# Optimization experiments

Hardware: AMD Instinct MI355X
Metric: run time of the kernel (lower is better)

The kernel has to match this reference:

```python
import jax, jax.numpy as jnp
import numpy as np

MARGIN = 0.5
EPS = 1e-6  # torch F.pairwise_distance adds eps to the difference before the norm
B, N, D = 1024, 1024, 64


def setup_inputs() -> dict:
    key = jax.random.key(0)
    ka, kp, kn = jax.random.split(key, 3)
    anchor = jax.random.normal(ka, (B, N, D), dtype=jnp.float32)
    positive = jax.random.normal(kp, (B, N, D), dtype=jnp.float32)
    negative = jax.random.normal(kn, (B, N, D), dtype=jnp.float32)
    return {"anchor": anchor, "positive": positive, "negative": negative}


def reference(anchor, positive, negative):
    # pairwise L2 distances over the feature dim -> [B, N]
    dist_pos = jnp.linalg.norm(anchor - positive + EPS, axis=-1)
    dist_neg = jnp.linalg.norm(anchor - negative + EPS, axis=-1)

    # hard-negative mining, vectorized over the batch:
    # candidates are columns where dist_pos - dist_neg + margin > 0;
    # among candidates pick the column with the LARGEST dist_neg
    diff = dist_pos - dist_neg + MARGIN            # [B, N]
    valid = diff > 0                               # [B, N]
    neg_scores = jnp.where(valid, dist_neg, -jnp.inf)
    sel_col = jnp.argmax(neg_scores, axis=1)       # [B] column index of hard negative

    # faithful to the original: negative is indexed on its FIRST dim with the
    # selected column index (requires B == N), yielding [B, N, D]
    hard_neg = negative[sel_col]
    has_valid = jnp.any(valid, axis=1)             # rows the original would keep

    loss = jnp.mean(jax.nn.relu(MARGIN + dist_pos - dist_neg))
    return loss, hard_neg, has_valid
```

## Files before the change

### kernel.cpp

```cpp
#include <hip/hip_runtime.h>
#include <math.h>

#define BB 1024
#define NN 1024
#define DD 64
#define MARGIN_V 0.5f
#define EPS_V 1e-6f
#define QSPLIT 8
#define QCOLS (NN / QSPLIT)

typedef float f32x4 __attribute__((ext_vector_type(4)));

__global__ __launch_bounds__(256) void k_dist(const float* __restrict__ a,
                                              const float* __restrict__ p,
                                              const float* __restrict__ g,
                                              float* __restrict__ ws_loss,
                                              float* __restrict__ ws_score,
                                              int* __restrict__ ws_idx,
                                              int* __restrict__ ws_valid)
{
    const int blk  = blockIdx.x;
    const int b    = blk >> 3;
    const int q    = blk & 7;
    const int tid  = threadIdx.x;
    const int lane = tid & 63;
    const int wave = tid >> 6;
    const int grp  = lane >> 4;
    const int gl   = lane & 15;
    const int group = wave * 4 + grp;

    const size_t base  = (size_t)b * (NN * DD);
    const int    ncol0 = q * QCOLS + group;
    const size_t off00 = base + (size_t)ncol0 * DD + (size_t)gl * 4;

    float loss_acc   = 0.f;
    float best_score = -INFINITY;
    int   best_idx   = 0;
    int   any_valid  = 0;

    f32x4 cA0 = __builtin_nontemporal_load((const f32x4*)(a + off00));
    f32x4 cP0 = __builtin_nontemporal_load((const f32x4*)(p + off00));
    f32x4 cG0 = *(const f32x4*)(g + off00);
    f32x4 cA1 = __builtin_nontemporal_load((const f32x4*)(a + off00 + 16 * DD));
    f32x4 cP1 = __builtin_nontemporal_load((const f32x4*)(p + off00 + 16 * DD));
    f32x4 cG1 = *(const f32x4*)(g + off00 + 16 * DD);

    #pragma unroll
    for (int j = 0; j < 4; ++j) {
        f32x4 nA0, nP0, nG0, nA1, nP1, nG1;
        if (j < 3) {
            const size_t offn = off00 + (size_t)((j + 1) * 32) * DD;
            nA0 = __builtin_nontemporal_load((const f32x4*)(a + offn));
            nP0 = __builtin_nontemporal_load((const f32x4*)(p + offn));
            nG0 = *(const f32x4*)(g + offn);
            nA1 = __builtin_nontemporal_load((const f32x4*)(a + offn + 16 * DD));
            nP1 = __builtin_nontemporal_load((const f32x4*)(p + offn + 16 * DD));
            nG1 = *(const f32x4*)(g + offn + 16 * DD);
        }

        const int n0 = ncol0 + j * 32;
        const int n1 = n0 + 16;

        float dp0 = 0.f, dn0 = 0.f, dp1 = 0.f, dn1 = 0.f, t;
        #pragma unroll
        for (int e = 0; e < 4; ++e) {
            t = cA0[e] - cP0[e] + EPS_V; dp0 += t * t;
            t = cA0[e] - cG0[e] + EPS_V; dn0 += t * t;
            t = cA1[e] - cP1[e] + EPS_V; dp1 += t * t;
            t = cA1[e] - cG1[e] + EPS_V; dn1 += t * t;
        }

        for (int m = 1; m < 16; m <<= 1) {
            dp0 += __shfl_xor(dp0, m, 64);
            dn0 += __shfl_xor(dn0, m, 64);
            dp1 += __shfl_xor(dp1, m, 64);
            dn1 += __shfl_xor(dn1, m, 64);
        }

        if (gl == 0) {
            {
                const float diff = MARGIN_V + sqrtf(dp0) - sqrtf(dn0);
                loss_acc += fmaxf(diff, 0.f);
                const bool valid = diff > 0.f;
                any_valid |= (int)valid;
                const float score = valid ? sqrtf(dn0) : -INFINITY;
                if (score > best_score) { best_score = score; best_idx = n0; }
            }
            {
                const float diff = MARGIN_V + sqrtf(dp1) - sqrtf(dn1);
                loss_acc += fmaxf(diff, 0.f);
                const bool valid = diff > 0.f;
                any_valid |= (int)valid;
                const float score = valid ? sqrtf(dn1) : -INFINITY;
                if (score > best_score) { best_score = score; best_idx = n1; }
            }
        }

        if (j < 3) {
            cA0 = nA0; cP0 = nP0; cG0 = nG0;
            cA1 = nA1; cP1 = nP1; cG1 = nG1;
        }
    }

    __shared__ float s_score[16];
    __shared__ int   s_idx[16];
    __shared__ float s_loss[16];
    __shared__ int   s_valid[16];
    if (gl == 0) {
        s_score[group] = best_score;
        s_idx[group]   = best_idx;
        s_loss[group]  = loss_acc;
        s_valid[group] = any_valid;
    }
    __syncthreads();
    if (tid == 0) {
        float bs = s_score[0]; int bi = s_idx[0];
        float ls = s_loss[0];  int av = s_valid[0];
        for (int k = 1; k < 16; ++k) {
            const float sc = s_score[k]; const int ix = s_idx[k];
            if (sc > bs || (sc == bs && ix < bi)) { bs = sc; bi = ix; }
            ls += s_loss[k];
            av |= s_valid[k];
        }
        ws_loss[blk]  = ls;
        ws_score[blk] = bs;
        ws_idx[blk]   = bi;
        ws_valid[blk] = av;
    }
}

__global__ __launch_bounds__(1024) void k_merge(const float* __restrict__ ws_loss,
                                                const float* __restrict__ ws_score,
                                                const int* __restrict__ ws_idx,
                                                const int* __restrict__ ws_valid,
                                                float* __restrict__ out_loss,
                                                int* __restrict__ ws_sel,
                                                float* __restrict__ out_hasvalid)
{
    const int b = threadIdx.x;
    float ls = 0.f;
    float bs = -INFINITY;
    int   bi = 0x7fffffff;
    int   av = 0;
    for (int qq = 0; qq < QSPLIT; ++qq) {
        const int idx = b * QSPLIT + qq;
        const float sc = ws_score[idx];
        const int   ix = ws_idx[idx];
        if (sc > bs || (sc == bs && ix < bi)) { bs = sc; bi = ix; }
        ls += ws_loss[idx];
        av |= ws_valid[idx];
    }
    ws_sel[b] = bi;
    out_hasvalid[b] = av ? 1.0f : 0.0f;

    __shared__ float s[16];
    float v = ls;
    for (int m = 1; m < 64; m <<= 1) v += __shfl_xor(v, m, 64);
    if ((b & 63) == 0) s[b >> 6] = v;
    __syncthreads();
    if (b == 0) {
        float tot = 0.f;
        for (int k = 0; k < 16; ++k) tot += s[k];
        out_loss[0] = tot / (float)((size_t)BB * NN);
    }
}

__global__ __launch_bounds__(256) void k_gather(const float* __restrict__ g,
                                                const int* __restrict__ ws_sel,
                                                float* __restrict__ out_hn)
{
    const int b   = blockIdx.y;
    const int sel = ws_sel[b];
    const float* __restrict__ src = g      + (size_t)sel * (NN * DD);
    float* __restrict__       dst = out_hn + (size_t)b   * (NN * DD);
    const int t = blockIdx.x * blockDim.x + threadIdx.x;
    #pragma unroll
    for (int k = 0; k < (NN * DD) / 8192; ++k) {
        const int idx = t + k * 8192;
        __builtin_nontemporal_store(src[idx], dst + idx);
    }
}

extern "C" void kernel_launch(void* const* d_in, const int* in_sizes, int n_in,
                              void* d_out, int out_size, void* d_ws, size_t ws_size,
                              hipStream_t stream) {
    const float* anchor   = (const float*)d_in[0];
    const float* positive = (const float*)d_in[1];
    const float* negative = (const float*)d_in[2];
    float* out = (float*)d_out;

    float* out_loss     = out;
    float* out_hard_neg = out + 1;
    float* out_hasvalid = out + 1 + (size_t)BB * NN * DD;

    float* ws_loss  = (float*)d_ws;
    float* ws_score = ws_loss + BB * QSPLIT;
    int*   ws_idx   = (int*)(ws_score + BB * QSPLIT);
    int*   ws_valid = ws_idx + BB * QSPLIT;
    int*   ws_sel   = ws_valid + BB * QSPLIT;

    k_dist<<<dim3(BB * QSPLIT), dim3(256), 0, stream>>>(anchor, positive, negative,
                                                        ws_loss, ws_score, ws_idx, ws_valid);
    k_merge<<<dim3(1), dim3(1024), 0, stream>>>(ws_loss, ws_score, ws_idx, ws_valid,
                                                out_loss, ws_sel, out_hasvalid);
    k_gather<<<dim3(32, BB), dim3(256), 0, stream>>>(negative, ws_sel, out_hard_neg);
}
```

Baseline: 223.2 us.

## Map one thread per column in distance kernel and halve the column split

The distance kernel now gives each thread one whole 64-float row. The thread reads that row with sixteen 16-byte loads and reduces it locally, where before a 16-lane group split the row and reduced it with shuffles. The split per batch row drops from 8 blocks to 4, and the argmax/loss reduction becomes a wave-wide shuffle reduction. The valid flag is now derived from the best score. The aim is to remove the per-column cross-lane shuffle work. The cost is that each load instruction now has lanes strided 256 bytes apart, which hurts coalescing in a kernel that is bound by memory bandwidth.

```diff
diff --git a/kernel.cpp b/kernel.cpp
--- a/kernel.cpp
+++ b/kernel.cpp
@@ -6,7 +6,7 @@
 #define DD 64
 #define MARGIN_V 0.5f
 #define EPS_V 1e-6f
-#define QSPLIT 8
+#define QSPLIT 4
 #define QCOLS (NN / QSPLIT)
 
 typedef float f32x4 __attribute__((ext_vector_type(4)));
@@ -19,113 +19,85 @@
                                               int* __restrict__ ws_idx,
                                               int* __restrict__ ws_valid)
 {
-    const int blk  = blockIdx.x;
-    const int b    = blk >> 3;
-    const int q    = blk & 7;
-    const int tid  = threadIdx.x;
-    const int lane = tid & 63;
-    const int wave = tid >> 6;
-    const int grp  = lane >> 4;
-    const int gl   = lane & 15;
-    const int group = wave * 4 + grp;
+    const int blk = blockIdx.x;
+    const int b   = blk >> 2;
+    const int q   = blk & 3;
+    const int tid = threadIdx.x;
+    const int n   = q * QCOLS + tid;
 
-    const size_t base  = (size_t)b * (NN * DD);
-    const int    ncol0 = q * QCOLS + group;
-    const size_t off00 = base + (size_t)ncol0 * DD + (size_t)gl * 4;
+    const float* pa = a + (size_t)b * (NN * DD) + (size_t)n * DD;
+    const float* pp = p + (size_t)b * (NN * DD) + (size_t)n * DD;
+    const float* pg = g + (size_t)b * (NN * DD) + (size_t)n * DD;
 
-    float loss_acc   = 0.f;
-    float best_score = -INFINITY;
-    int   best_idx   = 0;
-    int   any_valid  = 0;
-
-    f32x4 cA0 = __builtin_nontemporal_load((const f32x4*)(a + off00));
-    f32x4 cP0 = __builtin_nontemporal_load((const f32x4*)(p + off00));
-    f32x4 cG0 = *(const f32x4*)(g + off00);
-    f32x4 cA1 = __builtin_nontemporal_load((const f32x4*)(a + off00 + 16 * DD));
-    f32x4 cP1 = __builtin_nontemporal_load((const f32x4*)(p + off00 + 16 * DD));
-    f32x4 cG1 = *(const f32x4*)(g + off00 + 16 * DD);
+    float dp0 = 0.f, dp1 = 0.f, dn0 = 0.f, dn1 = 0.f;
 
     #pragma unroll
-    for (int j = 0; j < 4; ++j) {
-        f32x4 nA0, nP0, nG0, nA1, nP1, nG1;
-        if (j < 3) {
-            const size_t offn = off00 + (size_t)((j + 1) * 32) * DD;
-            nA0 = __builtin_nontemporal_load((const f32x4*)(a + offn));
-            nP0 = __builtin_nontemporal_load((const f32x4*)(p + offn));
-            nG0 = *(const f32x4*)(g + offn);
-            nA1 = __builtin_nontemporal_load((const f32x4*)(a + offn + 16 * DD));
-            nP1 = __builtin_nontemporal_load((const f32x4*)(p + offn + 16 * DD));
-            nG1 = *(const f32x4*)(g + offn + 16 * DD);
-        }
+    for (int c = 0; c < 4; ++c) {
+        f32x4 va[4], vp[4], vg[4];
+        #pragma unroll
+        for (int s = 0; s < 4; ++s)
+            va[s] = __builtin_nontemporal_load((const f32x4*)(pa + c * 16 + s * 4));
+        #pragma unroll
+        for (int s = 0; s < 4; ++s)
+            vp[s] = __builtin_nontemporal_load((const f32x4*)(pp + c * 16 + s * 4));
+        #pragma unroll
+        for (int s = 0; s < 4; ++s)
+            vg[s] = *(const f32x4*)(pg + c * 16 + s * 4);
 
-        const int n0 = ncol0 + j * 32;
-        const int n1 = n0 + 16;
-
-        float dp0 = 0.f, dn0 = 0.f, dp1 = 0.f, dn1 = 0.f, t;
+        float accp0 = 0.f, accp1 = 0.f, accn0 = 0.f, accn1 = 0.f, t;
         #pragma unroll
-        for (int e = 0; e < 4; ++e) {
-            t = cA0[e] - cP0[e] + EPS_V; dp0 += t * t;
-            t = cA0[e] - cG0[e] + EPS_V; dn0 += t * t;
-            t = cA1[e] - cP1[e] + EPS_V; dp1 += t * t;
-            t = cA1[e] - cG1[e] + EPS_V; dn1 += t * t;
-        }
-
-        for (int m = 1; m < 16; m <<= 1) {
-            dp0 += __shfl_xor(dp0, m, 64);
-            dn0 += __shfl_xor(dn0, m, 64);
-            dp1 += __shfl_xor(dp1, m, 64);
-            dn1 += __shfl_xor(dn1, m, 64);
-        }
-
-        if (gl == 0) {
-            {
-                const float diff = MARGIN_V + sqrtf(dp0) - sqrtf(dn0);
-                loss_acc += fmaxf(diff, 0.f);
-                const bool valid = diff > 0.f;
-                any_valid |= (int)valid;
-                const float score = valid ? sqrtf(dn0) : -INFINITY;
-                if (score > best_score) { best_score = score; best_idx = n0; }
-            }
-            {
-                const float diff = MARGIN_V + sqrtf(dp1) - sqrtf(dn1);
-                loss_acc += fmaxf(diff, 0.f);
-                const bool valid = diff > 0.f;
-                any_valid |= (int)valid;
-                const float score = valid ? sqrtf(dn1) : -INFINITY;
-                if (score > best_score) { best_score = score; best_idx = n1; }
+        for (int s = 0; s < 4; s += 2) {
+            #pragma unroll
+            for (int e = 0; e < 4; ++e) {
+                t = va[s][e]     - vp[s][e]     + EPS_V; accp0 += t * t;
+                t = va[s][e]     - vg[s][e]     + EPS_V; accn0 += t * t;
+                t = va[s + 1][e] - vp[s + 1][e] + EPS_V; accp1 += t * t;
+                t = va[s + 1][e] - vg[s + 1][e] + EPS_V; accn1 += t * t;
             }
         }
-
-        if (j < 3) {
-            cA0 = nA0; cP0 = nP0; cG0 = nG0;
-            cA1 = nA1; cP1 = nP1; cG1 = nG1;
-        }
+        dp0 += accp0; dp1 += accp1;
+        dn0 += accn0; dn1 += accn1;
     }
 
-    __shared__ float s_score[16];
-    __shared__ int   s_idx[16];
-    __shared__ float s_loss[16];
-    __shared__ int   s_valid[16];
-    if (gl == 0) {
-        s_score[group] = best_score;
-        s_idx[group]   = best_idx;
-        s_loss[group]  = loss_acc;
-        s_valid[group] = any_valid;
+    const float dpt = dp0 + dp1;
+    const float dnt = dn0 + dn1;
+
+    const float dist_pos = sqrtf(dpt);
+    const float dist_neg = sqrtf(dnt);
+    const float diff = MARGIN_V + dist_pos - dist_neg;
+    float loss  = fmaxf(diff, 0.f);
+    float score = (diff > 0.f) ? dist_neg : -INFINITY;
+    int   idx   = n;
+
+    for (int m = 1; m < 64; m <<= 1) {
+        loss += __shfl_xor(loss, m, 64);
+        const float so = __shfl_xor(score, m, 64);
+        const int   io = __shfl_xor(idx, m, 64);
+        if (so > score || (so == score && io < idx)) { score = so; idx = io; }
+    }
+
+    __shared__ float s_loss[4];
+    __shared__ float s_score[4];
+    __shared__ int   s_idx[4];
+    const int wave = tid >> 6;
+    if ((tid & 63) == 0) {
+        s_loss[wave]  = loss;
+        s_score[wave] = score;
+        s_idx[wave]   = idx;
     }
     __syncthreads();
     if (tid == 0) {
-        float bs = s_score[0]; int bi = s_idx[0];
-        float ls = s_loss[0];  int av = s_valid[0];
-        for (int k = 1; k < 16; ++k) {
+        float ls = 0.f, bs = -INFINITY;
+        int   bi = 0x7fffffff;
+        for (int k = 0; k < 4; ++k) {
+            ls += s_loss[k];
             const float sc = s_score[k]; const int ix = s_idx[k];
             if (sc > bs || (sc == bs && ix < bi)) { bs = sc; bi = ix; }
-            ls += s_loss[k];
-            av |= s_valid[k];
         }
         ws_loss[blk]  = ls;
         ws_score[blk] = bs;
         ws_idx[blk]   = bi;
-        ws_valid[blk] = av;
+        ws_valid[blk] = (bs > -INFINITY) ? 1 : 0;
     }
 }
 
```

After: 450.2 us. 102% more time.
